# Performance work log

Measured on AMD Instinct MI355X. Metric: run time of the kernel, lower is better.

## Reference

```python
import jax, jax.numpy as jnp
import numpy as np

B, S = 128, 512
VOCAB, E, H, T = 100000, 100, 128, 10  # tagset_size=10 -> CRF over T-1=9 tags
HD = H // 2  # per-direction LSTM hidden


def setup_inputs():
    key = jax.random.key(0)
    ks = jax.random.split(key, 14)
    s = 0.08
    inputs = jax.random.randint(ks[0], (B, S), 1, VOCAB)
    tags = jax.random.randint(ks[1], (B, S), 1, T)  # valid after tags-1 shift
    mask = jnp.ones((B, S), dtype=bool)
    emb = (jax.random.normal(ks[2], (VOCAB, E)) * s).at[0].set(0.0)  # padding_idx=0 row zeroed
    Wih_f = jax.random.normal(ks[3], (4 * HD, E)) * s
    Whh_f = jax.random.normal(ks[4], (4 * HD, HD)) * s
    b_f = jax.random.normal(ks[5], (4 * HD,)) * s
    Wih_b = jax.random.normal(ks[6], (4 * HD, E)) * s
    Whh_b = jax.random.normal(ks[7], (4 * HD, HD)) * s
    b_b = jax.random.normal(ks[8], (4 * HD,)) * s
    W_out = jax.random.normal(ks[9], (T, H)) * s
    b_out = jax.random.normal(ks[10], (T,)) * s
    start = jax.random.normal(ks[11], (T - 1,)) * s
    end = jax.random.normal(ks[12], (T - 1,)) * s
    trans = jax.random.normal(ks[13], (T - 1, T - 1)) * s
    return dict(inputs=inputs, tags=tags, mask=mask, emb=emb,
                Wih_f=Wih_f, Whh_f=Whh_f, b_f=b_f,
                Wih_b=Wih_b, Whh_b=Whh_b, b_b=b_b,
                W_out=W_out, b_out=b_out, start=start, end=end, trans=trans)


def _lstm_dir(x, Wih, Whh, b, reverse):
    # x: [S, B, E] time-major; PyTorch gate order i,f,g,o; b = b_ih + b_hh
    h0 = jnp.zeros((x.shape[1], Whh.shape[1]), x.dtype)

    def step(carry, xt):
        h, c = carry
        gates = xt @ Wih.T + h @ Whh.T + b
        i, f, g, o = jnp.split(gates, 4, axis=-1)
        c = jax.nn.sigmoid(f) * c + jax.nn.sigmoid(i) * jnp.tanh(g)
        h = jax.nn.sigmoid(o) * jnp.tanh(c)
        return (h, c), h

    _, hs = jax.lax.scan(step, (h0, h0), x, reverse=reverse)
    return hs  # [S, B, HD]


def _crf_nll(em, tags, mask, start, end, trans):
    # Linear-chain CRF (torchcrf-style). em: [S,B,K], tags/mask: [S,B]
    pick = lambda e, t: jnp.take_along_axis(e, t[:, None], axis=-1)[:, 0]
    # numerator: score of the gold path
    score0 = start[tags[0]] + pick(em[0], tags[0])

    def num_step(sc, inp):
        em_t, t, tp, m = inp
        return sc + jnp.where(m, trans[tp, t] + pick(em_t, t), 0.0), None

    score, _ = jax.lax.scan(num_step, score0, (em[1:], tags[1:], tags[:-1], mask[1:]))
    last_idx = mask.sum(0).astype(jnp.int32) - 1
    last_tags = jnp.take_along_axis(tags, last_idx[None, :], axis=0)[0]
    score = score + end[last_tags]
    # denominator: forward algorithm (log partition)
    alpha0 = start[None, :] + em[0]  # [B,K]

    def fwd_step(alpha, inp):
        em_t, m = inp
        nxt = jax.nn.logsumexp(alpha[:, :, None] + trans[None, :, :] + em_t[:, None, :], axis=1)
        return jnp.where(m[:, None], nxt, alpha), None

    alpha, _ = jax.lax.scan(fwd_step, alpha0, (em[1:], mask[1:]))
    logZ = jax.nn.logsumexp(alpha + end[None, :], axis=1)
    return -(score - logZ).mean()  # loss = -log_likelihood.mean()


def _forward(inputs, tags, mask, emb, Wih_f, Whh_f, b_f, Wih_b, Whh_b, b_b, W_out, b_out, start, end, trans):
    x = emb[inputs].transpose(1, 0, 2)  # [S,B,E]
    h = jnp.concatenate([_lstm_dir(x, Wih_f, Whh_f, b_f, False),
                         _lstm_dir(x, Wih_b, Whh_b, b_b, True)], axis=-1)  # [S,B,H]
    # dropout is identity at eval; slice off tag 0 as in the module
    em = (h @ W_out.T + b_out)[:, :, 1:]  # [S,B,T-1]
    return _crf_nll(em, (tags - 1).T, mask.T, start, end, trans)


def reference(inputs, tags, mask, emb, Wih_f, Whh_f, b_f, Wih_b, Whh_b, b_b, W_out, b_out, start, end, trans):
    return _forward(inputs, tags, mask, emb, Wih_f, Whh_f, b_f, Wih_b, Whh_b, b_b, W_out, b_out, start, end, trans)
```

## Files before the change

### kernel.cpp

```cpp
#include <hip/hip_runtime.h>
#include <math.h>

#define SB 512
#define NB 128
#define HD 64

typedef _Float16 h2 __attribute__((ext_vector_type(2)));
union U4 { uint4 u; h2 h[4]; _Float16 f[8]; };
union U2 { uint2 u; _Float16 f[4]; };
union UH { unsigned u; _Float16 f[2]; };

__device__ __forceinline__ float frcp(float x) { return __builtin_amdgcn_rcpf(x); }
__device__ __forceinline__ float fsig(float x) { return frcp(1.0f + __expf(-x)); }
__device__ __forceinline__ float ftanh(float x) {
    float t = __expf(-2.0f * fabsf(x));
    float r = (1.0f - t) * frcp(1.0f + t);
    return copysignf(r, x);
}
__device__ __forceinline__ float fdot2(h2 a, h2 b, float c) {
    return __builtin_amdgcn_fdot2(a, b, c, false);
}

__global__ void prep_kernel(const float* __restrict__ Wih_f, const float* __restrict__ Wih_bb,
                            const float* __restrict__ Whh_f, const float* __restrict__ Whh_bb,
                            const float* __restrict__ b_f, const float* __restrict__ b_bb,
                            const float* __restrict__ trans,
                            unsigned* __restrict__ W2h, unsigned* __restrict__ whh16,
                            float* __restrict__ bias2, float* __restrict__ Eexp)
{
    int idx = blockIdx.x * 256 + threadIdx.x;
    if (idx < 26624) {
        int col = idx / 52, d = idx - col * 52;
        int dir = col >> 8, r = col & 255, j = r >> 2, g = r & 3;
        const float* src = (dir ? Wih_bb : Wih_f) + (g * 64 + j) * 100;
        UH u; u.u = 0;
        if (d < 50) { u.f[0] = (_Float16)src[2 * d]; u.f[1] = (_Float16)src[2 * d + 1]; }
        W2h[idx] = u.u;
    } else if (idx < 43008) {
        int d = idx - 26624;
        int kp = d & 31, u = (d >> 5) & 63, g = (d >> 11) & 3, dir = d >> 13;
        const float* src = (dir ? Whh_bb : Whh_f) + (g * 64 + u) * 64 + 2 * kp;
        UH uu; uu.f[0] = (_Float16)src[0]; uu.f[1] = (_Float16)src[1];
        whh16[d] = uu.u;
    } else if (idx < 43520) {
        int col = idx - 43008;
        int dir = col >> 8, r = col & 255, j = r >> 2, g = r & 3;
        bias2[col] = (dir ? b_bb : b_f)[g * 64 + j];
    } else if (idx < 43601) {
        int i = idx - 43520;
        Eexp[i] = __expf(trans[i]);
    }
}

__global__ __launch_bounds__(256, 1) void gemm_kernel(
    const int* __restrict__ inputs, const float* __restrict__ emb,
    const unsigned* __restrict__ W2h, const float* __restrict__ bias2,
    _Float16* __restrict__ xgh)
{
    __shared__ __align__(16) unsigned sE[128 * 52];
    __shared__ __align__(16) unsigned sW[128 * 52];
    __shared__ int stok[128];
    const int bx = blockIdx.x;
    const int tt = bx >> 2;
    const int cb = (bx & 3) * 128;
    const int tid = threadIdx.x;

    if (tid < 128) stok[tid] = inputs[tid * SB + tt];
    for (int idx = tid; idx < 1664; idx += 256)
        ((uint4*)sW)[idx] = ((const uint4*)W2h)[cb * 13 + idx];
    __syncthreads();
    for (int idx = tid; idx < 6656; idx += 256) {
        int row = idx / 52, d = idx - row * 52;
        int token = stok[row];
        UH u; u.u = 0;
        if (d < 50) {
            const float* ep = emb + (size_t)token * 100 + 2 * d;
            u.f[0] = (_Float16)ep[0]; u.f[1] = (_Float16)ep[1];
        }
        sE[idx] = u.u;
    }
    __syncthreads();

    const int tx = tid & 15, ty = tid >> 4;
    float acc[8][8];
    #pragma unroll
    for (int r = 0; r < 8; ++r)
        #pragma unroll
        for (int i = 0; i < 8; ++i) acc[r][i] = 0.f;

    for (int kk = 0; kk < 13; ++kk) {
        U4 e[8], wv[8];
        #pragma unroll
        for (int r = 0; r < 8; ++r) e[r].u = ((const uint4*)sE)[(ty + 16 * r) * 13 + kk];
        #pragma unroll
        for (int i = 0; i < 8; ++i) wv[i].u = ((const uint4*)sW)[(tx + 16 * i) * 13 + kk];
        #pragma unroll
        for (int r = 0; r < 8; ++r)
            #pragma unroll
            for (int i = 0; i < 8; ++i) {
                float a = acc[r][i];
                #pragma unroll
                for (int q = 0; q < 4; ++q) a = fdot2(e[r].h[q], wv[i].h[q], a);
                acc[r][i] = a;
            }
    }

    #pragma unroll
    for (int i = 0; i < 8; ++i) {
        int col = cb + tx + 16 * i;
        float bc = bias2[col];
        #pragma unroll
        for (int r = 0; r < 8; ++r) {
            int row = tt * NB + ty + 16 * r;
            xgh[(size_t)row * 512 + col] = (_Float16)(acc[r][i] + bc);
        }
    }
}

__global__ __attribute__((amdgpu_flat_work_group_size(64, 64), amdgpu_waves_per_eu(1, 1)))
void lstm_kernel(
    const _Float16* __restrict__ xgh, const unsigned* __restrict__ whh16,
    _Float16* __restrict__ h16)
{
    const int blk = blockIdx.x;
    const int b = blk & (NB - 1);
    const int dir = blk >> 7;
    const int j = threadIdx.x;

    U4 w[32];
    const uint4* W4 = (const uint4*)(whh16 + dir * 8192);
    #pragma unroll
    for (int g = 0; g < 4; ++g)
        #pragma unroll
        for (int k4 = 0; k4 < 8; ++k4)
            w[g * 8 + k4].u = W4[(g * 64 + j) * 8 + k4];

    __shared__ __align__(16) _Float16 hbuf[64];
    hbuf[j] = (_Float16)0.f;
    float c = 0.f;

    const int t0 = dir ? (SB - 1) : 0;
    const ptrdiff_t xstride = (dir ? -1 : 1) * (ptrdiff_t)(NB * 512);
    const _Float16* xp = xgh + ((size_t)(t0 * NB + b)) * 512 + dir * 256 + j * 4;
    _Float16* hp = h16 + ((size_t)(b * 2 + dir) * SB + t0) * 64 + j;
    const ptrdiff_t hstride = (dir ? -1 : 1) * (ptrdiff_t)64;

    U2 p0, p1;
    p0.u = *(const uint2*)xp;
    p1.u = *(const uint2*)(xp + xstride);
    const _Float16* xq = xp + 2 * xstride;
    __syncthreads();

    for (int s = 0; s < SB; ++s) {
        float a0 = (float)p0.f[0], a1 = (float)p0.f[1];
        float a2 = (float)p0.f[2], a3 = (float)p0.f[3];
        p0 = p1;
        p1.u = *(const uint2*)xq;
        xq += xstride;

        U4 hv[8];
        #pragma unroll
        for (int k4 = 0; k4 < 8; ++k4) hv[k4].u = *(const uint4*)&hbuf[k4 * 8];

        float g0[4] = {a0, 0.f, 0.f, 0.f};
        float g1[4] = {a1, 0.f, 0.f, 0.f};
        float g2[4] = {a2, 0.f, 0.f, 0.f};
        float g3[4] = {a3, 0.f, 0.f, 0.f};
        #pragma unroll
        for (int k4 = 0; k4 < 8; ++k4) {
            const int p = k4 & 3;
            #pragma unroll
            for (int q = 0; q < 4; ++q) {
                g0[p] = fdot2(hv[k4].h[q], w[0 * 8 + k4].h[q], g0[p]);
                g1[p] = fdot2(hv[k4].h[q], w[1 * 8 + k4].h[q], g1[p]);
                g2[p] = fdot2(hv[k4].h[q], w[2 * 8 + k4].h[q], g2[p]);
                g3[p] = fdot2(hv[k4].h[q], w[3 * 8 + k4].h[q], g3[p]);
            }
        }
        a0 = (g0[0] + g0[1]) + (g0[2] + g0[3]);
        a1 = (g1[0] + g1[1]) + (g1[2] + g1[3]);
        a2 = (g2[0] + g2[1]) + (g2[2] + g2[3]);
        a3 = (g3[0] + g3[1]) + (g3[2] + g3[3]);

        float ig = fsig(a0), fg = fsig(a1), gg = ftanh(a2), og = fsig(a3);
        c = fg * c + ig * gg;
        float h = og * ftanh(c);
        *hp = (_Float16)h;
        hp += hstride;
        hbuf[j] = (_Float16)h;
    }
}

__global__ __launch_bounds__(256, 1) void proj_kernel(
    const _Float16* __restrict__ h16, const float* __restrict__ W_out,
    const float* __restrict__ b_out, float* __restrict__ em3)
{
    __shared__ __align__(16) unsigned tile[128 * 64];
    __shared__ __align__(16) unsigned sWo[9 * 64];
    __shared__ float sb[9];
    const int b = blockIdx.x, tid = threadIdx.x;

    for (int i2 = tid; i2 < 576; i2 += 256) {
        int k = i2 >> 6, jp = i2 & 63;
        const float* src = W_out + (k + 1) * 128 + 2 * jp;
        UH u; u.f[0] = (_Float16)src[0]; u.f[1] = (_Float16)src[1];
        sWo[i2] = u.u;
    }
    if (tid < 9) sb[tid] = b_out[1 + tid];

    float* dst0 = em3 + (size_t)b * (SB * 12);

    for (int tt = 0; tt < 4; ++tt) {
        const int t0 = tt * 128;
        __syncthreads();
        #pragma unroll
        for (int dir = 0; dir < 2; ++dir) {
            const unsigned* src = (const unsigned*)(h16 + ((size_t)(b * 2 + dir) * SB + t0) * 64);
            for (int i = tid; i < 4096; i += 256) {
                int t = i >> 5, jp = i & 31;
                tile[t * 64 + dir * 32 + jp] = src[i];
            }
        }
        __syncthreads();

        for (int o = tid; o < 1152; o += 256) {
            int tl = o / 9, k = o - 9 * tl;
            const U4* hr = (const U4*)&tile[tl * 64];
            const U4* wr = (const U4*)&sWo[k * 64];
            float pa = 0.f, pb = 0.f;
            #pragma unroll
            for (int q = 0; q < 16; q += 2) {
                U4 hv = hr[q], wv = wr[q];
                U4 hv2 = hr[q + 1], wv2 = wr[q + 1];
                #pragma unroll
                for (int z = 0; z < 4; ++z) {
                    pa = fdot2(hv.h[z], wv.h[z], pa);
                    pb = fdot2(hv2.h[z], wv2.h[z], pb);
                }
            }
            dst0[(t0 + tl) * 12 + k] = pa + pb + sb[k];
        }
    }
}

__global__ __launch_bounds__(64, 1) void crf_gold(
    const float* __restrict__ em3, const int* __restrict__ tags,
    const float* __restrict__ startv, const float* __restrict__ endv,
    const float* __restrict__ trans, float* __restrict__ gold)
{
    const int b = blockIdx.x, l = threadIdx.x;
    const int* tb = tags + (size_t)b * SB;
    const float* eb = em3 + (size_t)b * (SB * 12);
    float sc = 0.f;
    for (int t = l; t < SB; t += 64) {
        int tg = tb[t] - 1;
        if (t > 0) {
            int tp = tb[t - 1] - 1;
            sc += trans[tp * 9 + tg] + eb[t * 12 + tg];
        }
    }
    if (l == 0) {
        int tg0 = tb[0] - 1, tgl = tb[SB - 1] - 1;
        sc += startv[tg0] + eb[tg0] + endv[tgl];
    }
    #pragma unroll
    for (int off = 32; off > 0; off >>= 1) sc += __shfl_down(sc, off);
    if (l == 0) gold[b] = sc;
}

__global__ __launch_bounds__(256, 1) void crf_scan(
    const float* __restrict__ em3, const float* __restrict__ Eexp,
    float* __restrict__ Pws)
{
    const int lane = blockIdx.x * 256 + threadIdx.x;
    const int c = lane & 31, b = lane >> 5;

    float E[81];
    #pragma unroll
    for (int i = 0; i < 81; ++i) E[i] = Eexp[i];

    float P[81];
    #pragma unroll
    for (int i = 0; i < 81; ++i) P[i] = 0.f;
    #pragma unroll
    for (int i = 0; i < 9; ++i) P[i * 9 + i] = 1.f;
    float M = 0.f;

    const int t0 = 1 + 16 * c;
    const int nst = (t0 + 16 <= SB) ? 16 : (SB - t0);
    const float* ep = em3 + (size_t)b * (SB * 12) + t0 * 12;

    for (int s = 0; s < nst; ++s, ep += 12) {
        float4 e0 = *(const float4*)ep;
        float4 e1 = *(const float4*)(ep + 4);
        float e8 = ep[8];
        float ex[9] = { __expf(e0.x), __expf(e0.y), __expf(e0.z), __expf(e0.w),
                        __expf(e1.x), __expf(e1.y), __expf(e1.z), __expf(e1.w),
                        __expf(e8) };
        #pragma unroll
        for (int i = 0; i < 9; ++i) {
            float tmp[9];
            #pragma unroll
            for (int jj = 0; jj < 9; ++jj) tmp[jj] = P[i * 9] * E[jj];
            #pragma unroll
            for (int k = 1; k < 9; ++k)
                #pragma unroll
                for (int jj = 0; jj < 9; ++jj) tmp[jj] += P[i * 9 + k] * E[k * 9 + jj];
            #pragma unroll
            for (int jj = 0; jj < 9; ++jj) P[i * 9 + jj] = tmp[jj] * ex[jj];
        }
        if ((s & 3) == 3) {
            float mx = P[0];
            #pragma unroll
            for (int i = 1; i < 81; ++i) mx = fmaxf(mx, P[i]);
            M += __logf(mx);
            float r = frcp(mx);
            #pragma unroll
            for (int i = 0; i < 81; ++i) P[i] *= r;
        }
    }

    float* dst = Pws + (size_t)lane * 84;
    #pragma unroll
    for (int i = 0; i < 81; ++i) dst[i] = P[i];
    dst[81] = M;
}

__global__ __launch_bounds__(128, 1) void crf_combine(
    const float* __restrict__ em3, const float* __restrict__ Pws,
    const float* __restrict__ gold, const float* __restrict__ startv,
    const float* __restrict__ endv, float* __restrict__ out)
{
    const int b = threadIdx.x;
    float A[9], M = 0.f;
    {
        const float* eb = em3 + (size_t)b * (SB * 12);
        float4 e0 = *(const float4*)eb;
        float4 e1 = *(const float4*)(eb + 4);
        float e[9] = { e0.x, e0.y, e0.z, e0.w, e1.x, e1.y, e1.z, e1.w, eb[8] };
        #pragma unroll
        for (int k = 0; k < 9; ++k) A[k] = __expf(startv[k] + e[k]);
    }

    for (int c = 0; c < 32; ++c) {
        const float4* src = (const float4*)(Pws + ((size_t)b * 32 + c) * 84);
        float buf[84];
        #pragma unroll
        for (int q = 0; q < 21; ++q) {
            float4 v = src[q];
            buf[4 * q] = v.x; buf[4 * q + 1] = v.y; buf[4 * q + 2] = v.z; buf[4 * q + 3] = v.w;
        }
        float tmp[9];
        #pragma unroll
        for (int jj = 0; jj < 9; ++jj) tmp[jj] = A[0] * buf[jj];
        #pragma unroll
        for (int i = 1; i < 9; ++i)
            #pragma unroll
            for (int jj = 0; jj < 9; ++jj) tmp[jj] += A[i] * buf[i * 9 + jj];
        float mx = tmp[0];
        #pragma unroll
        for (int jj = 1; jj < 9; ++jj) mx = fmaxf(mx, tmp[jj]);
        M += __logf(mx) + buf[81];
        float r = frcp(mx);
        #pragma unroll
        for (int jj = 0; jj < 9; ++jj) A[jj] = tmp[jj] * r;
    }

    float Z = 0.f;
    #pragma unroll
    for (int k = 0; k < 9; ++k) Z += A[k] * __expf(endv[k]);
    float part = M + __logf(Z) - gold[b];

    #pragma unroll
    for (int off = 32; off > 0; off >>= 1) part += __shfl_down(part, off);
    __shared__ float sm[2];
    if ((b & 63) == 0) sm[b >> 6] = part;
    __syncthreads();
    if (b == 0) out[0] = (sm[0] + sm[1]) * (1.0f / NB);
}

extern "C" void kernel_launch(void* const* d_in, const int* in_sizes, int n_in,
                              void* d_out, int out_size, void* d_ws, size_t ws_size,
                              hipStream_t stream)
{
    const int*   inputs = (const int*)d_in[0];
    const int*   tags   = (const int*)d_in[1];
    const float* emb    = (const float*)d_in[3];
    const float* Wih_f  = (const float*)d_in[4];
    const float* Whh_f  = (const float*)d_in[5];
    const float* b_f    = (const float*)d_in[6];
    const float* Wih_b  = (const float*)d_in[7];
    const float* Whh_b  = (const float*)d_in[8];
    const float* b_b    = (const float*)d_in[9];
    const float* W_out  = (const float*)d_in[10];
    const float* b_out  = (const float*)d_in[11];
    const float* startv = (const float*)d_in[12];
    const float* endv   = (const float*)d_in[13];
    const float* transv = (const float*)d_in[14];

    char* w = (char*)d_ws;
    float* em3     = (float*)w;     w += (size_t)NB * SB * 12 * 4;
    _Float16* xgh  = (_Float16*)w;  w += (size_t)SB * NB * 512 * 2;
    _Float16* h16  = (_Float16*)w;  w += (size_t)NB * 2 * SB * 64 * 2;
    float* Pws     = (float*)w;     w += (size_t)NB * 32 * 84 * 4;
    float* gold    = (float*)w;     w += NB * 4;
    unsigned* W2h  = (unsigned*)w;  w += 26624 * 4;
    unsigned* whh16= (unsigned*)w;  w += 16384 * 4;
    float* bias2   = (float*)w;     w += 512 * 4;
    float* Eexp    = (float*)w;     w += 81 * 4;

    prep_kernel<<<171, 256, 0, stream>>>(Wih_f, Wih_b, Whh_f, Whh_b, b_f, b_b, transv,
                                         W2h, whh16, bias2, Eexp);
    gemm_kernel<<<2048, 256, 0, stream>>>(inputs, emb, W2h, bias2, xgh);
    lstm_kernel<<<256, 64, 0, stream>>>(xgh, whh16, h16);
    proj_kernel<<<NB, 256, 0, stream>>>(h16, W_out, b_out, em3);
    crf_gold<<<NB, 64, 0, stream>>>(em3, tags, startv, endv, transv, gold);
    crf_scan<<<16, 256, 0, stream>>>(em3, Eexp, Pws);
    crf_combine<<<1, 128, 0, stream>>>(em3, Pws, gold, startv, endv, (float*)d_out);
}
```

Before: 543.8 us.

## Reuse embedding tile across gate columns and stage LSTM recurrent weights in LDS

The input-projection GEMM now launches one block per timestep and loops over all four 128-column weight slices. The gathered embedding tile is therefore built once instead of four times, at the cost of fewer, longer blocks. In the LSTM kernel, the recurrent weights are relaid out in the prep kernel and staged in shared memory rather than held in 128 registers; each step re-reads them from LDS. The xgh prefetch is also deepened to three steps. This frees registers but adds LDS read latency to every step of the serial recurrence.

```diff
diff --git a/kernel.cpp b/kernel.cpp
--- a/kernel.cpp
+++ b/kernel.cpp
@@ -41,7 +41,8 @@
         int kp = d & 31, u = (d >> 5) & 63, g = (d >> 11) & 3, dir = d >> 13;
         const float* src = (dir ? Whh_bb : Whh_f) + (g * 64 + u) * 64 + 2 * kp;
         UH uu; uu.f[0] = (_Float16)src[0]; uu.f[1] = (_Float16)src[1];
-        whh16[d] = uu.u;
+        int k4 = kp >> 2, q = kp & 3;
+        whh16[(((dir * 4 + g) * 8 + k4) * 64 + u) * 4 + q] = uu.u;
     } else if (idx < 43520) {
         int col = idx - 43008;
         int dir = col >> 8, r = col & 255, j = r >> 2, g = r & 3;
@@ -60,14 +61,10 @@
     __shared__ __align__(16) unsigned sE[128 * 52];
     __shared__ __align__(16) unsigned sW[128 * 52];
     __shared__ int stok[128];
-    const int bx = blockIdx.x;
-    const int tt = bx >> 2;
-    const int cb = (bx & 3) * 128;
+    const int tt = blockIdx.x;
     const int tid = threadIdx.x;
 
     if (tid < 128) stok[tid] = inputs[tid * SB + tt];
-    for (int idx = tid; idx < 1664; idx += 256)
-        ((uint4*)sW)[idx] = ((const uint4*)W2h)[cb * 13 + idx];
     __syncthreads();
     for (int idx = tid; idx < 6656; idx += 256) {
         int row = idx / 52, d = idx - row * 52;
@@ -79,40 +76,48 @@
         }
         sE[idx] = u.u;
     }
-    __syncthreads();
 
     const int tx = tid & 15, ty = tid >> 4;
-    float acc[8][8];
-    #pragma unroll
-    for (int r = 0; r < 8; ++r)
-        #pragma unroll
-        for (int i = 0; i < 8; ++i) acc[r][i] = 0.f;
-
-    for (int kk = 0; kk < 13; ++kk) {
-        U4 e[8], wv[8];
-        #pragma unroll
-        for (int r = 0; r < 8; ++r) e[r].u = ((const uint4*)sE)[(ty + 16 * r) * 13 + kk];
-        #pragma unroll
-        for (int i = 0; i < 8; ++i) wv[i].u = ((const uint4*)sW)[(tx + 16 * i) * 13 + kk];
+
+    for (int cb4 = 0; cb4 < 4; ++cb4) {
+        const int cb = cb4 * 128;
+        __syncthreads();
+        for (int idx = tid; idx < 1664; idx += 256)
+            ((uint4*)sW)[idx] = ((const uint4*)W2h)[cb * 13 + idx];
+        __syncthreads();
+
+        float acc[8][8];
         #pragma unroll
         for (int r = 0; r < 8; ++r)
             #pragma unroll
-            for (int i = 0; i < 8; ++i) {
-                float a = acc[r][i];
+            for (int i = 0; i < 8; ++i) acc[r][i] = 0.f;
+
+        for (int kk = 0; kk < 13; ++kk) {
+            U4 e[8], wv[8];
+            #pragma unroll
+            for (int r = 0; r < 8; ++r) e[r].u = ((const uint4*)sE)[(ty + 16 * r) * 13 + kk];
+            #pragma unroll
+            for (int i = 0; i < 8; ++i) wv[i].u = ((const uint4*)sW)[(tx + 16 * i) * 13 + kk];
+            #pragma unroll
+            for (int r = 0; r < 8; ++r)
                 #pragma unroll
-                for (int q = 0; q < 4; ++q) a = fdot2(e[r].h[q], wv[i].h[q], a);
-                acc[r][i] = a;
+                for (int i = 0; i < 8; ++i) {
+                    float a = acc[r][i];
+                    #pragma unroll
+                    for (int q = 0; q < 4; ++q) a = fdot2(e[r].h[q], wv[i].h[q], a);
+                    acc[r][i] = a;
+                }
+        }
+
+        #pragma unroll
+        for (int i = 0; i < 8; ++i) {
+            int col = cb + tx + 16 * i;
+            float bc = bias2[col];
+            #pragma unroll
+            for (int r = 0; r < 8; ++r) {
+                int row = tt * NB + ty + 16 * r;
+                xgh[(size_t)row * 512 + col] = (_Float16)(acc[r][i] + bc);
             }
-    }
-
-    #pragma unroll
-    for (int i = 0; i < 8; ++i) {
-        int col = cb + tx + 16 * i;
-        float bc = bias2[col];
-        #pragma unroll
-        for (int r = 0; r < 8; ++r) {
-            int row = tt * NB + ty + 16 * r;
-            xgh[(size_t)row * 512 + col] = (_Float16)(acc[r][i] + bc);
         }
     }
 }
@@ -127,15 +132,15 @@
     const int dir = blk >> 7;
     const int j = threadIdx.x;
 
-    U4 w[32];
-    const uint4* W4 = (const uint4*)(whh16 + dir * 8192);
-    #pragma unroll
-    for (int g = 0; g < 4; ++g)
-        #pragma unroll
-        for (int k4 = 0; k4 < 8; ++k4)
-            w[g * 8 + k4].u = W4[(g * 64 + j) * 8 + k4];
-
+    __shared__ __align__(16) unsigned wlds[8192];
     __shared__ __align__(16) _Float16 hbuf[64];
+
+    {
+        const uint4* src = (const uint4*)(whh16 + dir * 8192);
+        uint4* dst = (uint4*)wlds;
+        #pragma unroll
+        for (int i = 0; i < 32; ++i) dst[i * 64 + j] = src[i * 64 + j];
+    }
     hbuf[j] = (_Float16)0.f;
     float c = 0.f;
 
@@ -145,17 +150,19 @@
     _Float16* hp = h16 + ((size_t)(b * 2 + dir) * SB + t0) * 64 + j;
     const ptrdiff_t hstride = (dir ? -1 : 1) * (ptrdiff_t)64;
 
-    U2 p0, p1;
+    U2 p0, p1, p2;
     p0.u = *(const uint2*)xp;
     p1.u = *(const uint2*)(xp + xstride);
-    const _Float16* xq = xp + 2 * xstride;
-    __syncthreads();
+    p2.u = *(const uint2*)(xp + 2 * xstride);
+    const _Float16* xq = xp + 3 * xstride;
+
+    const uint4* wl = (const uint4*)wlds;
 
     for (int s = 0; s < SB; ++s) {
         float a0 = (float)p0.f[0], a1 = (float)p0.f[1];
         float a2 = (float)p0.f[2], a3 = (float)p0.f[3];
-        p0 = p1;
-        p1.u = *(const uint2*)xq;
+        p0 = p1; p1 = p2;
+        p2.u = *(const uint2*)xq;
         xq += xstride;
 
         U4 hv[8];
@@ -168,13 +175,18 @@
         float g3[4] = {a3, 0.f, 0.f, 0.f};
         #pragma unroll
         for (int k4 = 0; k4 < 8; ++k4) {
+            U4 w0, w1, w2, w3;
+            w0.u = wl[(0 * 8 + k4) * 64 + j];
+            w1.u = wl[(1 * 8 + k4) * 64 + j];
+            w2.u = wl[(2 * 8 + k4) * 64 + j];
+            w3.u = wl[(3 * 8 + k4) * 64 + j];
             const int p = k4 & 3;
             #pragma unroll
             for (int q = 0; q < 4; ++q) {
-                g0[p] = fdot2(hv[k4].h[q], w[0 * 8 + k4].h[q], g0[p]);
-                g1[p] = fdot2(hv[k4].h[q], w[1 * 8 + k4].h[q], g1[p]);
-                g2[p] = fdot2(hv[k4].h[q], w[2 * 8 + k4].h[q], g2[p]);
-                g3[p] = fdot2(hv[k4].h[q], w[3 * 8 + k4].h[q], g3[p]);
+                g0[p] = fdot2(hv[k4].h[q], w0.h[q], g0[p]);
+                g1[p] = fdot2(hv[k4].h[q], w1.h[q], g1[p]);
+                g2[p] = fdot2(hv[k4].h[q], w2.h[q], g2[p]);
+                g3[p] = fdot2(hv[k4].h[q], w3.h[q], g3[p]);
             }
         }
         a0 = (g0[0] + g0[1]) + (g0[2] + g0[3]);
@@ -411,7 +423,7 @@
 
     prep_kernel<<<171, 256, 0, stream>>>(Wih_f, Wih_b, Whh_f, Whh_b, b_f, b_b, transv,
                                          W2h, whh16, bias2, Eexp);
-    gemm_kernel<<<2048, 256, 0, stream>>>(inputs, emb, W2h, bias2, xgh);
+    gemm_kernel<<<SB, 256, 0, stream>>>(inputs, emb, W2h, bias2, xgh);
     lstm_kernel<<<256, 64, 0, stream>>>(xgh, whh16, h16);
     proj_kernel<<<NB, 256, 0, stream>>>(h16, W_out, b_out, em3);
     crf_gold<<<NB, 64, 0, stream>>>(em3, tags, startv, endv, transv, gold);
```

Measured after the change: 526.8 us. 3.1% less time.
